# Kernel tuning notes

Hardware: AMD Instinct MI355X
Metric: run time of the kernel (lower is better)

The kernel has to match this reference:

```python
import jax, jax.numpy as jnp
import numpy as np

H = 16  # num heads
D = 64  # head dim


def rotate_half(x):
    h = x.shape[-1] // 2
    return jnp.concatenate([-x[..., h:], x[..., :h]], axis=-1)


def setup_inputs() -> dict:
    key = jax.random.key(0)
    ks = jax.random.split(key, 8)
    B, S, E = 2, 4096, 1024
    scale = 1.0 / np.sqrt(E)
    x = jax.random.normal(ks[0], (B, S, E), dtype=jnp.float32)
    Wq = jax.random.normal(ks[1], (E, E), dtype=jnp.float32) * scale
    Wk = jax.random.normal(ks[2], (E, E), dtype=jnp.float32) * scale
    Wv = jax.random.normal(ks[3], (E, E), dtype=jnp.float32) * scale
    Wg = jax.random.normal(ks[4], (E, E), dtype=jnp.float32) * scale
    Wo = jax.random.normal(ks[5], (E, E), dtype=jnp.float32) * scale
    cos = jax.random.normal(ks[6], (S, D), dtype=jnp.float32)
    sin = jax.random.normal(ks[7], (S, D), dtype=jnp.float32)
    return {"x": x, "Wq": Wq, "Wk": Wk, "Wv": Wv, "Wg": Wg, "Wo": Wo,
            "cos": cos, "sin": sin, "block_size": 256}


def reference(x, Wq, Wk, Wv, Wg, Wo, cos, sin, block_size):
    B, S, E = x.shape
    nb = S // block_size  # seq divisible by block_size (remainder==0 path)

    gate = (x @ Wg).reshape(B, S, H, D)
    q = (x @ Wq).reshape(B, S, H, D)
    k = (x @ Wk).reshape(B, S, H, D)
    v = (x @ Wv).reshape(B, S, H, D)

    # RoPE: cos/sin [S, D] -> broadcast over batch and heads (unsqueeze_dim=1 in torch
    # with [S, 1, D] after slicing gives the same broadcast over the head axis here).
    c = cos[:S][None, :, None, :]  # [1, S, 1, D]
    s = sin[:S][None, :, None, :]
    q = q * c + rotate_half(q) * s
    k = k * c + rotate_half(k) * s

    # Block-diagonal attention: reshape seq into blocks and attend within blocks only.
    def to_blocks(t):  # [B,S,H,D] -> [B,nb,H,block,D]
        return t.reshape(B, nb, block_size, H, D).transpose(0, 1, 3, 2, 4)

    qb, kb, vb = to_blocks(q), to_blocks(k), to_blocks(v)
    scores = jnp.einsum('bnhqd,bnhkd->bnhqk', qb, kb) / np.sqrt(D)
    attn = jax.nn.softmax(scores, axis=-1)
    ob = jnp.einsum('bnhqk,bnhkd->bnhqd', attn, vb)

    out = ob.transpose(0, 1, 3, 2, 4).reshape(B, S, H, D)  # back to [B,S,H,D]
    out = (out * jax.nn.sigmoid(gate)).reshape(B, S, H * D)
    return out @ Wo
```

## Files before the change

### kernel.cpp

```cpp
#include <hip/hip_runtime.h>
#include <hip/hip_bf16.h>
#include <stdint.h>

typedef __bf16 bf16_t;
typedef __bf16 bf16x8 __attribute__((ext_vector_type(8)));
typedef float f32x4 __attribute__((ext_vector_type(4)));

#define DEVI __device__ __forceinline__

constexpr int BB = 2;
constexpr int SS = 4096;
constexpr int EE = 1024;
constexpr int HH = 16;
constexpr int DD = 64;
constexpr int MM = BB * SS;

DEVI void gload16(const void* g, void* l) {
  __builtin_amdgcn_global_load_lds(
      (const __attribute__((address_space(1))) void*)g,
      (__attribute__((address_space(3))) void*)l, 16, 0, 0);
}

__global__ void cvt_kernel(const float* __restrict__ in, bf16_t* __restrict__ out, int n8) {
  int i = blockIdx.x * 256 + threadIdx.x;
  if (i >= n8) return;
  const float* p = in + (size_t)i * 8;
  bf16x8 o;
#pragma unroll
  for (int j = 0; j < 8; ++j) o[j] = (bf16_t)p[j];
  *(bf16x8*)(out + (size_t)i * 8) = o;
}

__global__ void wt_kernel(const float* __restrict__ w0, const float* __restrict__ w1,
                          const float* __restrict__ w2, const float* __restrict__ w3,
                          const float* __restrict__ w4, bf16_t* __restrict__ out) {
  __shared__ float tile[32][33];
  const float* Wsel = blockIdx.z == 0 ? w0 : blockIdx.z == 1 ? w1 :
                      blockIdx.z == 2 ? w2 : blockIdx.z == 3 ? w3 : w4;
  bf16_t* O = out + (size_t)blockIdx.z * EE * EE;
  int n0 = blockIdx.x * 32, k0 = blockIdx.y * 32;
  int tx = threadIdx.x & 31, ty = threadIdx.x >> 5;
#pragma unroll
  for (int i = 0; i < 4; ++i)
    tile[ty + i * 8][tx] = Wsel[(size_t)(k0 + ty + i * 8) * EE + n0 + tx];
  __syncthreads();
#pragma unroll
  for (int i = 0; i < 4; ++i)
    O[(size_t)(n0 + ty + i * 8) * EE + k0 + tx] = (bf16_t)tile[tx][ty + i * 8];
}

__global__ __launch_bounds__(512, 2) void gemm8p(const bf16_t* __restrict__ A,
                                                 const bf16_t* __restrict__ Bt,
                                                 bf16_t* __restrict__ Obase,
                                                 const float* __restrict__ cosp,
                                                 const float* __restrict__ sinp) {
  __shared__ bf16_t Al[2][2][128][64];
  __shared__ bf16_t Bl[2][2][128][64];
  const int id = blockIdx.x;
  const int swz = (id & 7) * 64 + (id >> 3);
  const int bx = swz >> 4, by = swz & 15;
  const int m0 = bx << 8, n0 = by << 8;
  const int tid = threadIdx.x, wv = tid >> 6, ln = tid & 63;
  const int wm = wv >> 2, wn = wv & 3;
  const int sr = tid >> 3;
  const int scs = (tid & 7) ^ (sr & 7);
  const bf16_t* Abase = A + ((size_t)(m0 + sr) << 10) + scs * 8;
  const bf16_t* Bbase = Bt + ((size_t)(n0 + sr) << 10) + scs * 8;

  f32x4 acc[8][4] = {};
  bf16x8 bfr[4][2];

#define STA(BUFI, H, J, KT) \
  gload16(Abase + (((H)*128 + (J)*64) << 10) + (KT)*64, &Al[BUFI][H][(J)*64 + wv * 8][0])
#define STB(BUFI, H, J, KT) \
  gload16(Bbase + (((H)*128 + (J)*64) << 10) + (KT)*64, &Bl[BUFI][H][(J)*64 + wv * 8][0])

#define PHASE(BUFI, MH, KK, LDB, STAGEC, WAITC) do {                           \
    bf16x8 af_[4];                                                             \
    _Pragma("unroll") for (int mi_ = 0; mi_ < 4; ++mi_) {                      \
      int ar_ = (MH)*64 + mi_*16 + (ln & 15);                                  \
      int ach_ = ((KK)*4 + (ln >> 4)) ^ (ar_ & 7);                             \
      af_[mi_] = *(const bf16x8*)&Al[BUFI][wm][ar_][ach_ * 8];                 \
    }                                                                          \
    if (LDB) {                                                                 \
      _Pragma("unroll") for (int ni_ = 0; ni_ < 4; ++ni_) {                    \
        int br_ = (wn & 1)*64 + ni_*16 + (ln & 15);                            \
        int bch_ = ((KK)*4 + (ln >> 4)) ^ (br_ & 7);                           \
        bfr[ni_][KK] = *(const bf16x8*)&Bl[BUFI][wn >> 1][br_][bch_ * 8];      \
      }                                                                        \
    }                                                                          \
    STAGEC;                                                                    \
    WAITC;                                                                     \
    __builtin_amdgcn_s_barrier();                                              \
    asm volatile("s_waitcnt lgkmcnt(0)" ::: "memory");                         \
    __builtin_amdgcn_s_setprio(1);                                             \
    _Pragma("unroll") for (int mi_ = 0; mi_ < 4; ++mi_)                        \
      _Pragma("unroll") for (int ni_ = 0; ni_ < 4; ++ni_)                      \
        acc[(MH)*4 + mi_][ni_] = __builtin_amdgcn_mfma_f32_16x16x32_bf16(      \
            af_[mi_], bfr[ni_][KK], acc[(MH)*4 + mi_][ni_], 0, 0, 0);          \
    __builtin_amdgcn_s_setprio(0);                                             \
    __builtin_amdgcn_s_barrier();                                              \
    asm volatile("" ::: "memory");                                             \
  } while (0)

  STA(0, 0, 0, 0); STA(0, 0, 1, 0); STA(0, 1, 0, 0); STA(0, 1, 1, 0);
  STB(0, 0, 0, 0); STB(0, 0, 1, 0); STB(0, 1, 0, 0); STB(0, 1, 1, 0);
  STB(1, 0, 0, 1); STB(1, 0, 1, 1); STB(1, 1, 0, 1); STB(1, 1, 1, 1);
  asm volatile("s_waitcnt vmcnt(4)" ::: "memory");
  __builtin_amdgcn_s_barrier();
  asm volatile("" ::: "memory");

#pragma unroll 1
  for (int i = 0; i < 8; ++i) {
    const int to = 2 * i + 1;
    PHASE(0, 0, 0, 1, ({ STA(1, 0, 0, to); STA(1, 0, 1, to); }), ((void)0));
    PHASE(0, 0, 1, 1, ({ STA(1, 1, 0, to); STA(1, 1, 1, to); }), ((void)0));
    PHASE(0, 1, 0, 0, ({ if (i < 7) { STB(0, 0, 0, to + 1); STB(0, 0, 1, to + 1); } }),
          ((void)0));
    PHASE(0, 1, 1, 0, ({ if (i < 7) { STB(0, 1, 0, to + 1); STB(0, 1, 1, to + 1); } }),
          ({ if (i < 7) { asm volatile("s_waitcnt vmcnt(4)" ::: "memory"); }
             else       { asm volatile("s_waitcnt vmcnt(0)" ::: "memory"); } }));
    PHASE(1, 0, 0, 1, ({ if (i < 7) { STA(0, 0, 0, to + 1); STA(0, 0, 1, to + 1); } }),
          ((void)0));
    PHASE(1, 0, 1, 1, ({ if (i < 7) { STA(0, 1, 0, to + 1); STA(0, 1, 1, to + 1); } }),
          ((void)0));
    PHASE(1, 1, 0, 0, ({ if (i < 7) { STB(1, 0, 0, to + 2); STB(1, 0, 1, to + 2); } }),
          ((void)0));
    PHASE(1, 1, 1, 0, ({ if (i < 7) { STB(1, 1, 0, to + 2); STB(1, 1, 1, to + 2); } }),
          ({ if (i < 7) { asm volatile("s_waitcnt vmcnt(4)" ::: "memory"); } }));
  }
#undef PHASE
#undef STA
#undef STB

  const int widx = n0 >> 10;
  const int cb = (n0 & 1023) + wn * 64;
  bf16_t* W = Obase + (size_t)widx * MM * EE;
  if (widx <= 1) {
#pragma unroll
    for (int mi = 0; mi < 8; ++mi) {
#pragma unroll
      for (int r = 0; r < 4; ++r) {
        int row = m0 + wm * 128 + mi * 16 + ((ln >> 4) << 2) + r;
        int s = row & (SS - 1);
        float cv[4], sv[4];
#pragma unroll
        for (int ni = 0; ni < 4; ++ni) {
          int d = ni * 16 + (ln & 15);
          cv[ni] = cosp[s * DD + d];
          sv[ni] = sinp[s * DD + d];
        }
#pragma unroll
        for (int ni = 0; ni < 4; ++ni) {
          float v = acc[mi][ni][r], p = acc[mi][ni ^ 2][r];
          float o = v * cv[ni] + (ni < 2 ? -p : p) * sv[ni];
          W[(size_t)row * EE + cb + ni * 16 + (ln & 15)] = (bf16_t)o;
        }
      }
    }
  } else if (widx == 2) {
#pragma unroll
    for (int mi = 0; mi < 8; ++mi)
#pragma unroll
      for (int ni = 0; ni < 4; ++ni) {
        int row = m0 + wm * 128 + mi * 16 + ((ln >> 4) << 2);
        int ncol = cb + ni * 16 + (ln & 15);
        int h = ncol >> 6, d = ncol & 63;
        int b = row >> 12, s = row & (SS - 1);
        bf16_t* p = W + (((size_t)b * HH + h) * DD + d) * SS + s;
#pragma unroll
        for (int r = 0; r < 4; ++r) p[r] = (bf16_t)acc[mi][ni][r];
      }
  } else {
#pragma unroll
    for (int mi = 0; mi < 8; ++mi)
#pragma unroll
      for (int ni = 0; ni < 4; ++ni) {
        int row = m0 + wm * 128 + mi * 16 + ((ln >> 4) << 2);
        int ncol = cb + ni * 16 + (ln & 15);
        bf16_t* p = W + (size_t)row * EE + ncol;
#pragma unroll
        for (int r = 0; r < 4; ++r) p[(size_t)r * EE] = (bf16_t)acc[mi][ni][r];
      }
  }
}

__global__ __launch_bounds__(256) void gemm_out(const bf16_t* __restrict__ A,
                                                const bf16_t* __restrict__ Bt,
                                                float* __restrict__ O) {
  __shared__ bf16_t Al[128 * 64];
  __shared__ bf16_t Bl[128 * 64];
  const int m0 = blockIdx.x * 128;
  const int n0 = blockIdx.y * 128;
  const int tid = threadIdx.x;
  const int wv = tid >> 6, ln = tid & 63;
  const int wm = wv >> 1, wn = wv & 1;
  f32x4 acc[4][4] = {};

  for (int k0 = 0; k0 < EE; k0 += 64) {
    __syncthreads();
#pragma unroll
    for (int i = 0; i < 4; ++i) {
      int slot = i * 256 + wv * 64 + ln;
      int r = slot >> 3, c = slot & 7;
      int cs = c ^ (r & 7);
      gload16(A + (size_t)(m0 + r) * EE + k0 + cs * 8, Al + (size_t)(i * 256 + wv * 64) * 8);
      gload16(Bt + (size_t)(n0 + r) * EE + k0 + cs * 8, Bl + (size_t)(i * 256 + wv * 64) * 8);
    }
    __syncthreads();
#pragma unroll
    for (int kk = 0; kk < 2; ++kk) {
      bf16x8 af[4], bfr[4];
#pragma unroll
      for (int mi = 0; mi < 4; ++mi) {
        int row = wm * 64 + mi * 16 + (ln & 15);
        int ch = (kk * 4 + (ln >> 4)) ^ (row & 7);
        af[mi] = *(const bf16x8*)(Al + row * 64 + ch * 8);
      }
#pragma unroll
      for (int ni = 0; ni < 4; ++ni) {
        int row = wn * 64 + ni * 16 + (ln & 15);
        int ch = (kk * 4 + (ln >> 4)) ^ (row & 7);
        bfr[ni] = *(const bf16x8*)(Bl + row * 64 + ch * 8);
      }
#pragma unroll
      for (int mi = 0; mi < 4; ++mi)
#pragma unroll
        for (int ni = 0; ni < 4; ++ni)
          acc[mi][ni] = __builtin_amdgcn_mfma_f32_16x16x32_bf16(af[mi], bfr[ni], acc[mi][ni], 0, 0, 0);
    }
  }

#pragma unroll
  for (int mi = 0; mi < 4; ++mi)
#pragma unroll
    for (int ni = 0; ni < 4; ++ni) {
      int row = m0 + wm * 64 + mi * 16 + ((ln >> 4) << 2);
      int col = n0 + wn * 64 + ni * 16 + (ln & 15);
#pragma unroll
      for (int r = 0; r < 4; ++r) O[(size_t)(row + r) * EE + col] = acc[mi][ni][r];
    }
}

__global__ __launch_bounds__(256) void attn_kernel(const bf16_t* __restrict__ Q,
                                                   const bf16_t* __restrict__ Kc,
                                                   const bf16_t* __restrict__ Vt,
                                                   const bf16_t* __restrict__ G,
                                                   bf16_t* __restrict__ AO) {
  __shared__ bf16_t Kl[2][64 * 64];
  __shared__ bf16_t Vl[2][64 * 64];
  __shared__ bf16_t Pl[4][64 * 64];
  const int bx = blockIdx.x;
  const int h = bx & 15, sb = (bx >> 4) & 15, b = bx >> 8;
  const int tid = threadIdx.x, wv = tid >> 6, ln = tid & 63;
  const int qrow0 = b * SS + sb * 256 + wv * 64;

  bf16x8 qf[4][2];
#pragma unroll
  for (int mi = 0; mi < 4; ++mi)
#pragma unroll
    for (int kk = 0; kk < 2; ++kk)
      qf[mi][kk] = *(const bf16x8*)(Q + (size_t)(qrow0 + mi * 16 + (ln & 15)) * EE +
                                    h * DD + kk * 32 + ((ln >> 4) << 3));

  f32x4 o[4][4] = {};
  float mr[4][4], lr[4][4];
#pragma unroll
  for (int i = 0; i < 4; ++i)
#pragma unroll
    for (int r = 0; r < 4; ++r) { mr[i][r] = -1e30f; lr[i][r] = 0.f; }

#define STAGE_KV(KC, BI) do {                                                        \
    const int krow0_ = b * SS + sb * 256 + (KC) * 64;                                \
    _Pragma("unroll") for (int i_ = 0; i_ < 2; ++i_) {                               \
      int slot_ = i_ * 256 + wv * 64 + ln;                                           \
      int r_ = slot_ >> 3, c_ = slot_ & 7, cs_ = c_ ^ (r_ & 7);                      \
      gload16(Kc + (size_t)(krow0_ + r_) * EE + h * DD + cs_ * 8,                    \
              &Kl[BI][(i_ * 256 + wv * 64) * 8]);                                    \
      gload16(Vt + (((size_t)b * HH + h) * DD + r_) * SS + sb * 256 + (KC) * 64 +    \
                  cs_ * 8,                                                           \
              &Vl[BI][(i_ * 256 + wv * 64) * 8]);                                    \
    }                                                                                \
  } while (0)

  STAGE_KV(0, 0);
  __syncthreads();

  for (int kc = 0; kc < 4; ++kc) {
    const int cur = kc & 1;
    if (kc < 3) STAGE_KV(kc + 1, cur ^ 1);

    f32x4 sc[4][4] = {};
    __builtin_amdgcn_s_setprio(1);
#pragma unroll
    for (int kk = 0; kk < 2; ++kk) {
      bf16x8 kf[4];
#pragma unroll
      for (int ni = 0; ni < 4; ++ni) {
        int row = ni * 16 + (ln & 15);
        int ch = (kk * 4 + (ln >> 4)) ^ (row & 7);
        kf[ni] = *(const bf16x8*)(&Kl[cur][row * 64 + ch * 8]);
      }
#pragma unroll
      for (int mi = 0; mi < 4; ++mi)
#pragma unroll
        for (int ni = 0; ni < 4; ++ni)
          sc[mi][ni] = __builtin_amdgcn_mfma_f32_16x16x32_bf16(qf[mi][kk], kf[ni], sc[mi][ni], 0, 0, 0);
    }
    __builtin_amdgcn_s_setprio(0);
#pragma unroll
    for (int mi = 0; mi < 4; ++mi)
#pragma unroll
      for (int ni = 0; ni < 4; ++ni) sc[mi][ni] *= 0.125f;

#pragma unroll
    for (int mi = 0; mi < 4; ++mi) {
#pragma unroll
      for (int r = 0; r < 4; ++r) {
        float mx = fmaxf(fmaxf(sc[mi][0][r], sc[mi][1][r]), fmaxf(sc[mi][2][r], sc[mi][3][r]));
#pragma unroll
        for (int d = 1; d < 16; d <<= 1) mx = fmaxf(mx, __shfl_xor(mx, d));
        float mn = fmaxf(mr[mi][r], mx);
        float scal = __expf(mr[mi][r] - mn);
        mr[mi][r] = mn;
        float rs = 0.f;
#pragma unroll
        for (int ni = 0; ni < 4; ++ni) {
          float p = __expf(sc[mi][ni][r] - mn);
          sc[mi][ni][r] = p;
          rs += p;
        }
#pragma unroll
        for (int d = 1; d < 16; d <<= 1) rs += __shfl_xor(rs, d);
        lr[mi][r] = lr[mi][r] * scal + rs;
#pragma unroll
        for (int nd = 0; nd < 4; ++nd) o[mi][nd][r] *= scal;
      }
    }

    bf16_t* P = Pl[wv];
#pragma unroll
    for (int mi = 0; mi < 4; ++mi)
#pragma unroll
      for (int ni = 0; ni < 4; ++ni)
#pragma unroll
        for (int r = 0; r < 4; ++r) {
          int row = mi * 16 + ((ln >> 4) << 2) + r;
          int col = ni * 16 + (ln & 15);
          P[row * 64 + (col ^ ((row & 7) << 3))] = (bf16_t)sc[mi][ni][r];
        }
    __builtin_amdgcn_s_setprio(1);
#pragma unroll
    for (int kk = 0; kk < 2; ++kk) {
      bf16x8 pf[4], vf[4];
#pragma unroll
      for (int mi = 0; mi < 4; ++mi) {
        int row = mi * 16 + (ln & 15);
        int ch = (kk * 4 + (ln >> 4)) ^ (row & 7);
        pf[mi] = *(const bf16x8*)(P + row * 64 + ch * 8);
      }
#pragma unroll
      for (int nd = 0; nd < 4; ++nd) {
        int row = nd * 16 + (ln & 15);
        int ch = (kk * 4 + (ln >> 4)) ^ (row & 7);
        vf[nd] = *(const bf16x8*)(&Vl[cur][row * 64 + ch * 8]);
      }
#pragma unroll
      for (int mi = 0; mi < 4; ++mi)
#pragma unroll
        for (int nd = 0; nd < 4; ++nd)
          o[mi][nd] = __builtin_amdgcn_mfma_f32_16x16x32_bf16(pf[mi], vf[nd], o[mi][nd], 0, 0, 0);
    }
    __builtin_amdgcn_s_setprio(0);
    __syncthreads();
  }
#undef STAGE_KV

#pragma unroll
  for (int mi = 0; mi < 4; ++mi)
#pragma unroll
    for (int nd = 0; nd < 4; ++nd)
#pragma unroll
      for (int r = 0; r < 4; ++r) {
        int m = qrow0 + mi * 16 + ((ln >> 4) << 2) + r;
        int col = h * DD + nd * 16 + (ln & 15);
        float gv = (float)G[(size_t)m * EE + col];
        float sig = 1.f / (1.f + __expf(-gv));
        AO[(size_t)m * EE + col] = (bf16_t)((o[mi][nd][r] / lr[mi][r]) * sig);
      }
}

extern "C" void kernel_launch(void* const* d_in, const int* in_sizes, int n_in,
                              void* d_out, int out_size, void* d_ws, size_t ws_size,
                              hipStream_t stream) {
  const float* x = (const float*)d_in[0];
  const float* Wq = (const float*)d_in[1];
  const float* Wk = (const float*)d_in[2];
  const float* Wv = (const float*)d_in[3];
  const float* Wg = (const float*)d_in[4];
  const float* Wo = (const float*)d_in[5];
  const float* cosp = (const float*)d_in[6];
  const float* sinp = (const float*)d_in[7];
  float* out = (float*)d_out;

  char* ws = (char*)d_ws;
  bf16_t* XB = (bf16_t*)(ws);
  bf16_t* WT = (bf16_t*)(ws + (16ll << 20));
  bf16_t* QB = (bf16_t*)(ws + (26ll << 20));
  bf16_t* KB = (bf16_t*)(ws + (42ll << 20));
  bf16_t* VT = (bf16_t*)(ws + (58ll << 20));
  bf16_t* GB = (bf16_t*)(ws + (74ll << 20));
  bf16_t* AO = XB;

  const int n8 = MM * EE / 8;
  cvt_kernel<<<n8 / 256, 256, 0, stream>>>(x, XB, n8);
  wt_kernel<<<dim3(32, 32, 5), 256, 0, stream>>>(Wq, Wk, Wv, Wg, Wo, WT);
  gemm8p<<<512, 512, 0, stream>>>(XB, WT, QB, cosp, sinp);
  attn_kernel<<<BB * (SS / 256) * HH, 256, 0, stream>>>(QB, KB, VT, GB, AO);
  gemm_out<<<dim3(MM / 128, EE / 128), 256, 0, stream>>>(AO, WT + (size_t)4 * EE * EE, out);
}
```

Before: 177.1 us.

## Replace pipelined 256x256 QKVG GEMM with simple 128x128 templated GEMM

```diff
diff --git a/kernel.cpp b/kernel.cpp
--- a/kernel.cpp
+++ b/kernel.cpp
@@ -49,145 +49,12 @@
     O[(size_t)(n0 + ty + i * 8) * EE + k0 + tx] = (bf16_t)tile[tx][ty + i * 8];
 }
 
-__global__ __launch_bounds__(512, 2) void gemm8p(const bf16_t* __restrict__ A,
-                                                 const bf16_t* __restrict__ Bt,
-                                                 bf16_t* __restrict__ Obase,
-                                                 const float* __restrict__ cosp,
-                                                 const float* __restrict__ sinp) {
-  __shared__ bf16_t Al[2][2][128][64];
-  __shared__ bf16_t Bl[2][2][128][64];
-  const int id = blockIdx.x;
-  const int swz = (id & 7) * 64 + (id >> 3);
-  const int bx = swz >> 4, by = swz & 15;
-  const int m0 = bx << 8, n0 = by << 8;
-  const int tid = threadIdx.x, wv = tid >> 6, ln = tid & 63;
-  const int wm = wv >> 2, wn = wv & 3;
-  const int sr = tid >> 3;
-  const int scs = (tid & 7) ^ (sr & 7);
-  const bf16_t* Abase = A + ((size_t)(m0 + sr) << 10) + scs * 8;
-  const bf16_t* Bbase = Bt + ((size_t)(n0 + sr) << 10) + scs * 8;
-
-  f32x4 acc[8][4] = {};
-  bf16x8 bfr[4][2];
-
-#define STA(BUFI, H, J, KT) \
-  gload16(Abase + (((H)*128 + (J)*64) << 10) + (KT)*64, &Al[BUFI][H][(J)*64 + wv * 8][0])
-#define STB(BUFI, H, J, KT) \
-  gload16(Bbase + (((H)*128 + (J)*64) << 10) + (KT)*64, &Bl[BUFI][H][(J)*64 + wv * 8][0])
-
-#define PHASE(BUFI, MH, KK, LDB, STAGEC, WAITC) do {                           \
-    bf16x8 af_[4];                                                             \
-    _Pragma("unroll") for (int mi_ = 0; mi_ < 4; ++mi_) {                      \
-      int ar_ = (MH)*64 + mi_*16 + (ln & 15);                                  \
-      int ach_ = ((KK)*4 + (ln >> 4)) ^ (ar_ & 7);                             \
-      af_[mi_] = *(const bf16x8*)&Al[BUFI][wm][ar_][ach_ * 8];                 \
-    }                                                                          \
-    if (LDB) {                                                                 \
-      _Pragma("unroll") for (int ni_ = 0; ni_ < 4; ++ni_) {                    \
-        int br_ = (wn & 1)*64 + ni_*16 + (ln & 15);                            \
-        int bch_ = ((KK)*4 + (ln >> 4)) ^ (br_ & 7);                           \
-        bfr[ni_][KK] = *(const bf16x8*)&Bl[BUFI][wn >> 1][br_][bch_ * 8];      \
-      }                                                                        \
-    }                                                                          \
-    STAGEC;                                                                    \
-    WAITC;                                                                     \
-    __builtin_amdgcn_s_barrier();                                              \
-    asm volatile("s_waitcnt lgkmcnt(0)" ::: "memory");                         \
-    __builtin_amdgcn_s_setprio(1);                                             \
-    _Pragma("unroll") for (int mi_ = 0; mi_ < 4; ++mi_)                        \
-      _Pragma("unroll") for (int ni_ = 0; ni_ < 4; ++ni_)                      \
-        acc[(MH)*4 + mi_][ni_] = __builtin_amdgcn_mfma_f32_16x16x32_bf16(      \
-            af_[mi_], bfr[ni_][KK], acc[(MH)*4 + mi_][ni_], 0, 0, 0);          \
-    __builtin_amdgcn_s_setprio(0);                                             \
-    __builtin_amdgcn_s_barrier();                                              \
-    asm volatile("" ::: "memory");                                             \
-  } while (0)
-
-  STA(0, 0, 0, 0); STA(0, 0, 1, 0); STA(0, 1, 0, 0); STA(0, 1, 1, 0);
-  STB(0, 0, 0, 0); STB(0, 0, 1, 0); STB(0, 1, 0, 0); STB(0, 1, 1, 0);
-  STB(1, 0, 0, 1); STB(1, 0, 1, 1); STB(1, 1, 0, 1); STB(1, 1, 1, 1);
-  asm volatile("s_waitcnt vmcnt(4)" ::: "memory");
-  __builtin_amdgcn_s_barrier();
-  asm volatile("" ::: "memory");
-
-#pragma unroll 1
-  for (int i = 0; i < 8; ++i) {
-    const int to = 2 * i + 1;
-    PHASE(0, 0, 0, 1, ({ STA(1, 0, 0, to); STA(1, 0, 1, to); }), ((void)0));
-    PHASE(0, 0, 1, 1, ({ STA(1, 1, 0, to); STA(1, 1, 1, to); }), ((void)0));
-    PHASE(0, 1, 0, 0, ({ if (i < 7) { STB(0, 0, 0, to + 1); STB(0, 0, 1, to + 1); } }),
-          ((void)0));
-    PHASE(0, 1, 1, 0, ({ if (i < 7) { STB(0, 1, 0, to + 1); STB(0, 1, 1, to + 1); } }),
-          ({ if (i < 7) { asm volatile("s_waitcnt vmcnt(4)" ::: "memory"); }
-             else       { asm volatile("s_waitcnt vmcnt(0)" ::: "memory"); } }));
-    PHASE(1, 0, 0, 1, ({ if (i < 7) { STA(0, 0, 0, to + 1); STA(0, 0, 1, to + 1); } }),
-          ((void)0));
-    PHASE(1, 0, 1, 1, ({ if (i < 7) { STA(0, 1, 0, to + 1); STA(0, 1, 1, to + 1); } }),
-          ((void)0));
-    PHASE(1, 1, 0, 0, ({ if (i < 7) { STB(1, 0, 0, to + 2); STB(1, 0, 1, to + 2); } }),
-          ((void)0));
-    PHASE(1, 1, 1, 0, ({ if (i < 7) { STB(1, 1, 0, to + 2); STB(1, 1, 1, to + 2); } }),
-          ({ if (i < 7) { asm volatile("s_waitcnt vmcnt(4)" ::: "memory"); } }));
-  }
-#undef PHASE
-#undef STA
-#undef STB
-
-  const int widx = n0 >> 10;
-  const int cb = (n0 & 1023) + wn * 64;
-  bf16_t* W = Obase + (size_t)widx * MM * EE;
-  if (widx <= 1) {
-#pragma unroll
-    for (int mi = 0; mi < 8; ++mi) {
-#pragma unroll
-      for (int r = 0; r < 4; ++r) {
-        int row = m0 + wm * 128 + mi * 16 + ((ln >> 4) << 2) + r;
-        int s = row & (SS - 1);
-        float cv[4], sv[4];
-#pragma unroll
-        for (int ni = 0; ni < 4; ++ni) {
-          int d = ni * 16 + (ln & 15);
-          cv[ni] = cosp[s * DD + d];
-          sv[ni] = sinp[s * DD + d];
-        }
-#pragma unroll
-        for (int ni = 0; ni < 4; ++ni) {
-          float v = acc[mi][ni][r], p = acc[mi][ni ^ 2][r];
-          float o = v * cv[ni] + (ni < 2 ? -p : p) * sv[ni];
-          W[(size_t)row * EE + cb + ni * 16 + (ln & 15)] = (bf16_t)o;
-        }
-      }
-    }
-  } else if (widx == 2) {
-#pragma unroll
-    for (int mi = 0; mi < 8; ++mi)
-#pragma unroll
-      for (int ni = 0; ni < 4; ++ni) {
-        int row = m0 + wm * 128 + mi * 16 + ((ln >> 4) << 2);
-        int ncol = cb + ni * 16 + (ln & 15);
-        int h = ncol >> 6, d = ncol & 63;
-        int b = row >> 12, s = row & (SS - 1);
-        bf16_t* p = W + (((size_t)b * HH + h) * DD + d) * SS + s;
-#pragma unroll
-        for (int r = 0; r < 4; ++r) p[r] = (bf16_t)acc[mi][ni][r];
-      }
-  } else {
-#pragma unroll
-    for (int mi = 0; mi < 8; ++mi)
-#pragma unroll
-      for (int ni = 0; ni < 4; ++ni) {
-        int row = m0 + wm * 128 + mi * 16 + ((ln >> 4) << 2);
-        int ncol = cb + ni * 16 + (ln & 15);
-        bf16_t* p = W + (size_t)row * EE + ncol;
-#pragma unroll
-        for (int r = 0; r < 4; ++r) p[(size_t)r * EE] = (bf16_t)acc[mi][ni][r];
-      }
-  }
-}
-
-__global__ __launch_bounds__(256) void gemm_out(const bf16_t* __restrict__ A,
-                                                const bf16_t* __restrict__ Bt,
-                                                float* __restrict__ O) {
+template <int MODE>
+__global__ __launch_bounds__(256) void gemm_bt(const bf16_t* __restrict__ A,
+                                               const bf16_t* __restrict__ Bt,
+                                               void* __restrict__ Cout,
+                                               const float* __restrict__ cosp,
+                                               const float* __restrict__ sinp) {
   __shared__ bf16_t Al[128 * 64];
   __shared__ bf16_t Bl[128 * 64];
   const int m0 = blockIdx.x * 128;
@@ -231,15 +98,68 @@
     }
   }
 
-#pragma unroll
-  for (int mi = 0; mi < 4; ++mi)
-#pragma unroll
-    for (int ni = 0; ni < 4; ++ni) {
-      int row = m0 + wm * 64 + mi * 16 + ((ln >> 4) << 2);
-      int col = n0 + wn * 64 + ni * 16 + (ln & 15);
-#pragma unroll
-      for (int r = 0; r < 4; ++r) O[(size_t)(row + r) * EE + col] = acc[mi][ni][r];
-    }
+  if (MODE == 0) {
+    const int widx = n0 >> 10;
+    const int cb = (n0 & 1023) + wn * 64;
+    bf16_t* W = (bf16_t*)Cout + (size_t)widx * MM * EE;
+    if (widx <= 1) {
+#pragma unroll
+      for (int mi = 0; mi < 4; ++mi) {
+#pragma unroll
+        for (int r = 0; r < 4; ++r) {
+          int row = m0 + wm * 64 + mi * 16 + ((ln >> 4) << 2) + r;
+          int s = row & (SS - 1);
+          float cv[4], sv[4];
+#pragma unroll
+          for (int ni = 0; ni < 4; ++ni) {
+            int d = ni * 16 + (ln & 15);
+            cv[ni] = cosp[s * DD + d];
+            sv[ni] = sinp[s * DD + d];
+          }
+#pragma unroll
+          for (int ni = 0; ni < 4; ++ni) {
+            float v = acc[mi][ni][r], p = acc[mi][ni ^ 2][r];
+            float o = v * cv[ni] + (ni < 2 ? -p : p) * sv[ni];
+            W[(size_t)row * EE + cb + ni * 16 + (ln & 15)] = (bf16_t)o;
+          }
+        }
+      }
+    } else if (widx == 2) {
+#pragma unroll
+      for (int mi = 0; mi < 4; ++mi)
+#pragma unroll
+        for (int ni = 0; ni < 4; ++ni) {
+          int row = m0 + wm * 64 + mi * 16 + ((ln >> 4) << 2);
+          int ncol = cb + ni * 16 + (ln & 15);
+          int h = ncol >> 6, d = ncol & 63;
+          int b = row >> 12, s = row & (SS - 1);
+          bf16_t* p = W + (((size_t)b * HH + h) * DD + d) * SS + s;
+#pragma unroll
+          for (int r = 0; r < 4; ++r) p[r] = (bf16_t)acc[mi][ni][r];
+        }
+    } else {
+#pragma unroll
+      for (int mi = 0; mi < 4; ++mi)
+#pragma unroll
+        for (int ni = 0; ni < 4; ++ni) {
+          int row = m0 + wm * 64 + mi * 16 + ((ln >> 4) << 2);
+          bf16_t* p = W + (size_t)row * EE + cb + ni * 16 + (ln & 15);
+#pragma unroll
+          for (int r = 0; r < 4; ++r) p[(size_t)r * EE] = (bf16_t)acc[mi][ni][r];
+        }
+    }
+  } else {
+    float* O = (float*)Cout;
+#pragma unroll
+    for (int mi = 0; mi < 4; ++mi)
+#pragma unroll
+      for (int ni = 0; ni < 4; ++ni) {
+        int row = m0 + wm * 64 + mi * 16 + ((ln >> 4) << 2);
+        int col = n0 + wn * 64 + ni * 16 + (ln & 15);
+#pragma unroll
+        for (int r = 0; r < 4; ++r) O[(size_t)(row + r) * EE + col] = acc[mi][ni][r];
+      }
+  }
 }
 
 __global__ __launch_bounds__(256) void attn_kernel(const bf16_t* __restrict__ Q,
@@ -415,7 +335,8 @@
   const int n8 = MM * EE / 8;
   cvt_kernel<<<n8 / 256, 256, 0, stream>>>(x, XB, n8);
   wt_kernel<<<dim3(32, 32, 5), 256, 0, stream>>>(Wq, Wk, Wv, Wg, Wo, WT);
-  gemm8p<<<512, 512, 0, stream>>>(XB, WT, QB, cosp, sinp);
+  gemm_bt<0><<<dim3(MM / 128, 4 * EE / 128), 256, 0, stream>>>(XB, WT, QB, cosp, sinp);
   attn_kernel<<<BB * (SS / 256) * HH, 256, 0, stream>>>(QB, KB, VT, GB, AO);
-  gemm_out<<<dim3(MM / 128, EE / 128), 256, 0, stream>>>(AO, WT + (size_t)4 * EE * EE, out);
-}
+  gemm_bt<1><<<dim3(MM / 128, EE / 128), 256, 0, stream>>>(AO, WT + (size_t)4 * EE * EE, out,
+                                                           nullptr, nullptr);
+}
```

Measured after the change: 190.8 us. 7.8% more time.
